# Kernel optimization log

Hardware: AMD Instinct MI355X
Metric: run time of the kernel (lower is better)

The kernel has to match this reference:

```python
import jax, jax.numpy as jnp
import numpy as np

B, S, D, H = 2, 2048, 1024, 16
HD = D // H


def setup_inputs() -> dict:
    key = jax.random.key(0)
    ks = jax.random.split(key, 5)
    scale = 0.02
    x = jax.random.normal(ks[0], (B, S, D), dtype=jnp.float32)
    Wq = jax.random.normal(ks[1], (D, D), dtype=jnp.float32) * scale
    Wk = jax.random.normal(ks[2], (D, D), dtype=jnp.float32) * scale
    Wv = jax.random.normal(ks[3], (D, D), dtype=jnp.float32) * scale
    Wo = jax.random.normal(ks[4], (D, D), dtype=jnp.float32) * scale
    z = jnp.zeros((D,), dtype=jnp.float32)
    return {"x": x, "Wq": Wq, "bq": z, "Wk": Wk, "bk": z, "Wv": Wv, "bv": z, "Wo": Wo, "bo": z}


def reference(x, Wq, bq, Wk, bk, Wv, bv, Wo, bo):
    b, s, d = x.shape
    hd = d // H
    # QKV projections -> [b, H, s, hd]
    def heads(W, bias):
        return (x @ W.T + bias).reshape(b, s, H, hd).transpose(0, 2, 1, 3)
    q = heads(Wq, bq)
    k = heads(Wk, bk)
    v = heads(Wv, bv)
    scale = 1.0 / np.sqrt(hd).astype(np.float32)
    attn = scale * jnp.einsum('bhqd,bhkd->bhqk', q, k)  # [b,H,s,s]
    # causal mask (attn dropout p=0 is identity before masking)
    causal = jnp.tril(jnp.ones((s, s), dtype=bool))
    attn = jnp.where(causal[None, None], attn, -jnp.inf)
    attn = jax.nn.softmax(attn, axis=-1)
    ans = jnp.einsum('bhqk,bhkd->bhqd', attn, v)
    ans = ans.transpose(0, 2, 1, 3).reshape(b, s, d)
    return ans @ Wo.T + bo
```

## Files before the change

### kernel.cpp

```cpp
#include <hip/hip_runtime.h>

#define DEV __device__ __forceinline__

typedef __attribute__((ext_vector_type(8))) __bf16 bf16x8;
typedef __attribute__((ext_vector_type(4))) float f32x4;
typedef __attribute__((ext_vector_type(16))) float f32x16;
typedef __attribute__((ext_vector_type(4))) unsigned short u16x4;
typedef __attribute__((ext_vector_type(8))) unsigned short u16x8;
typedef __attribute__((ext_vector_type(2))) unsigned u32x2;

DEV unsigned short f2bf(float f) {
  unsigned u = __builtin_bit_cast(unsigned, f);
  u += 0x7FFFu + ((u >> 16) & 1u);
  return (unsigned short)(u >> 16);
}

DEV f32x4 mfma16(bf16x8 a, bf16x8 b, f32x4 c) {
  return __builtin_amdgcn_mfma_f32_16x16x32_bf16(a, b, c, 0, 0, 0);
}
DEV f32x16 mfma32(bf16x8 a, bf16x8 b, f32x16 c) {
  return __builtin_amdgcn_mfma_f32_32x32x16_bf16(a, b, c, 0, 0, 0);
}

DEV void gload16(const void* g, void* l) {
  __builtin_amdgcn_global_load_lds(
      (const __attribute__((address_space(1))) unsigned int*)g,
      (__attribute__((address_space(3))) unsigned int*)l, 16, 0, 0);
}

DEV void plswap(unsigned& x, unsigned& y) {
#if __has_builtin(__builtin_amdgcn_permlane32_swap)
  u32x2 r = __builtin_amdgcn_permlane32_swap(x, y, false, false);
  x = r[0];
  y = r[1];
#else
  unsigned sx = __shfl_xor(x, 32, 64), sy = __shfl_xor(y, 32, 64);
  int hi = (threadIdx.x & 63) >> 5;
  unsigned nx = hi ? sy : x;
  unsigned ny = hi ? y : sx;
  x = nx;
  y = ny;
#endif
}
DEV float xadd32(float v) {
  unsigned a = __builtin_bit_cast(unsigned, v), b = a;
  plswap(a, b);
  return __builtin_bit_cast(float, a) + __builtin_bit_cast(float, b);
}

__global__ __launch_bounds__(256) void k_cvt_all(
    const float* __restrict__ x,
    const float* __restrict__ Wq, const float* __restrict__ Wk,
    const float* __restrict__ Wv, const float* __restrict__ Wo,
    unsigned short* __restrict__ xb,
    unsigned short* __restrict__ Wqb, unsigned short* __restrict__ Wkb,
    unsigned short* __restrict__ Wvb, unsigned short* __restrict__ Wob) {
  int g = blockIdx.x * 256 + threadIdx.x;
  const float* src;
  unsigned short* dst;
  int loc;
  if (g < 524288) {
    src = x; dst = xb; loc = g;
  } else {
    int r = g - 524288;
    int w = r >> 17;
    loc = r & 131071;
    src = w == 0 ? Wq : w == 1 ? Wk : w == 2 ? Wv : Wo;
    dst = w == 0 ? Wqb : w == 1 ? Wkb : w == 2 ? Wvb : Wob;
  }
  int row = loc >> 7, k8 = loc & 127;
  const f32x4* s = (const f32x4*)(src + ((size_t)row << 10) + (k8 << 3));
  f32x4 a = s[0], b = s[1];
  u16x8 o;
  o[0] = f2bf(a[0]); o[1] = f2bf(a[1]); o[2] = f2bf(a[2]); o[3] = f2bf(a[3]);
  o[4] = f2bf(b[0]); o[5] = f2bf(b[1]); o[6] = f2bf(b[2]); o[7] = f2bf(b[3]);
  *(u16x8*)(dst + ((size_t)row << 10) + ((k8 << 3) ^ ((row & 7) << 3))) = o;
}

DEV void gemm_mainloop(const char* Ag, const char* Bg, char* lds,
                       int lane, int wid, f32x4 acc[4][4]) {
  int g4 = lane >> 4, r16 = lane & 15;
  int wm = wid >> 1, wn = wid & 1;
  int adA[2], adB[2];
#pragma unroll
  for (int ks = 0; ks < 2; ++ks) {
    int swz = ((ks * 4 + g4) ^ (lane & 7)) << 4;
    adA[ks] = (wm * 64 + r16) * 128 + swz;
    adB[ks] = 16384 + (wn * 64 + r16) * 128 + swz;
  }
  int o0 = wid * 4096 + lane * 16;
  int grow[4], ginr[4];
#pragma unroll
  for (int i = 0; i < 4; ++i) {
    grow[i] = (o0 + i * 1024) >> 7;
    ginr[i] = (o0 + i * 1024) & 127;
  }
  auto STAGE = [&](int KT, int BASE) {
#pragma unroll
    for (int i = 0; i < 4; ++i) {
      int oo = o0 + i * 1024;
      size_t gofs = (size_t)grow[i] * 2048 + (size_t)KT * 128 + ginr[i];
      gload16(Ag + gofs, lds + BASE + oo);
      gload16(Bg + gofs, lds + BASE + 16384 + oo);
    }
  };
  STAGE(0, 0);
  __syncthreads();
  for (int kt = 0; kt < 16; ++kt) {
    int cur = (kt & 1) << 15;
    if (kt + 1 < 16) STAGE(kt + 1, cur ^ 32768);
#pragma unroll
    for (int ks = 0; ks < 2; ++ks) {
      bf16x8 af[4], bfr[4];
#pragma unroll
      for (int i = 0; i < 4; ++i) {
        af[i]  = *(const bf16x8*)(lds + cur + adA[ks] + i * 2048);
        bfr[i] = *(const bf16x8*)(lds + cur + adB[ks] + i * 2048);
      }
#pragma unroll
      for (int mi = 0; mi < 4; ++mi)
#pragma unroll
        for (int ni = 0; ni < 4; ++ni)
          acc[mi][ni] = mfma16(af[mi], bfr[ni], acc[mi][ni]);
    }
    __syncthreads();
  }
}

__global__ __launch_bounds__(256) void k_gemm_qkv(
    const unsigned short* __restrict__ xb,
    const unsigned short* __restrict__ Wqb, const unsigned short* __restrict__ Wkb,
    const unsigned short* __restrict__ Wvb,
    const float* __restrict__ bq, const float* __restrict__ bk,
    const float* __restrict__ bv,
    unsigned short* __restrict__ Qb, unsigned short* __restrict__ Kb,
    unsigned short* __restrict__ Vt) {
  __shared__ char lds[65536];
  int tid = threadIdx.x, lane = tid & 63, wid = tid >> 6;
  int bm = blockIdx.x & 31, bn = blockIdx.x >> 5;
  int r0 = bm * 128;
  int colT = bn * 128;
  int which = colT >> 10;
  int ncol = colT & 1023;
  const unsigned short* Wb = which == 0 ? Wqb : which == 1 ? Wkb : Wvb;
  f32x4 acc[4][4] = {};
  gemm_mainloop((const char*)xb + (size_t)r0 * 2048,
                (const char*)Wb + (size_t)ncol * 2048, lds, lane, wid, acc);
  int g4 = lane >> 4, r16 = lane & 15, wm = wid >> 1, wn = wid & 1;
  const float* bias = which == 0 ? bq : which == 1 ? bk : bv;
  int ncolw = ncol + wn * 64;
#pragma unroll
  for (int ni = 0; ni < 4; ++ni) {
    int gcol = ncolw + ni * 16 + r16;
    float bvv = bias[gcol];
    int h = gcol >> 6, hd = gcol & 63;
#pragma unroll
    for (int mi = 0; mi < 4; ++mi) {
      int growb = r0 + wm * 64 + mi * 16 + g4 * 4;
      int bb = growb >> 11, s0 = growb & 2047;
      if (which == 2) {
        u16x4 pk;
#pragma unroll
        for (int jj = 0; jj < 4; ++jj) pk[jj] = f2bf(acc[mi][ni][jj] + bvv);
        *(u16x4*)(Vt + ((size_t)(bb * 16 + h) * 64 + hd) * 2048 + s0) = pk;
      } else {
        unsigned short* dst = which == 0 ? Qb : Kb;
        size_t base = ((size_t)(bb * 16 + h) * 2048 + s0) * 64 + hd;
#pragma unroll
        for (int jj = 0; jj < 4; ++jj)
          dst[base + (size_t)jj * 64] = f2bf(acc[mi][ni][jj] + bvv);
      }
    }
  }
}

__global__ __launch_bounds__(256) void k_attn(
    const unsigned short* __restrict__ Q, const unsigned short* __restrict__ K,
    const unsigned short* __restrict__ Vt, unsigned short* __restrict__ ansb) {
  __shared__ char lds[3 * 16384 + 512];
  const float SCL = 0.18033688f;
  int tid = threadIdx.x, lane = tid & 63, wid = tid >> 6;
  int l31 = lane & 31, hi = lane >> 5;
  int bid = blockIdx.x;
  int bh = (bid & 7) * 4 + ((bid >> 3) & 3);
  int g = bid >> 5;
  int chunk = g < 8 ? 15 - g : g - 8;
  int b = bh >> 4, h = bh & 15;
  int q0 = chunk * 128 + wid * 32;
  int nt = 2 * chunk + 2;
  const unsigned short* Qh = Q + (size_t)bh * (2048 * 64);
  const char* Kg = (const char*)(K + (size_t)bh * (2048 * 64));
  const char* Vg = (const char*)(Vt + (size_t)bh * (64 * 2048));
  char* wb = lds + 49152 + wid * 128;

  int ldo0 = tid * 16, ldo1 = tid * 16 + 4096;
  int row0 = ldo0 >> 7, c0 = ldo0 & 127;
  int row1 = ldo1 >> 7, c1 = ldo1 & 127;
  int sc0 = c0 ^ ((row0 & 7) << 4), sc1 = c1 ^ ((row1 & 7) << 4);
  int ko0 = row0 * 128 + sc0, ko1 = row1 * 128 + sc1;
  int vo0 = row0 * 4096 + sc0, vo1 = row1 * 4096 + sc1;

  bf16x8 qf[4];
#pragma unroll
  for (int ks = 0; ks < 4; ++ks)
    qf[ks] = *(const bf16x8*)(Qh + (size_t)(q0 + l31) * 64 + ks * 16 + hi * 8);
  asm volatile("s_waitcnt vmcnt(0)" ::: "memory");

  f32x16 O0 = {}, O1 = {}, l16 = {};
  int swzl = (l31 & 7) << 4;
  int hioff = hi * 16;

  gload16(Kg + ko0, lds + ldo0);
  gload16(Kg + ko1, lds + ldo1);
  gload16(Vg + vo0, lds + 8192 + ldo0);
  gload16(Vg + vo1, lds + 8192 + ldo1);
  gload16(Kg + (size_t)64 * 128 + ko0, lds + 16384 + ldo0);
  gload16(Kg + (size_t)64 * 128 + ko1, lds + 16384 + ldo1);
  gload16(Vg + (size_t)64 * 2 + vo0, lds + 16384 + 8192 + ldo0);
  gload16(Vg + (size_t)64 * 2 + vo1, lds + 16384 + 8192 + ldo1);

  int cur = 0;
  for (int t = 0; t < nt; ++t) {
    if (t + 1 < nt) {
      asm volatile("s_waitcnt vmcnt(8)" ::: "memory");
    } else {
      asm volatile("s_waitcnt vmcnt(0)" ::: "memory");
    }
    __builtin_amdgcn_s_barrier();
    __builtin_amdgcn_sched_barrier(0);
    if (t + 2 < nt) {
      size_t kv2 = (size_t)(t + 2) * 64;
      int pb = (cur + 2 >= 3 ? cur - 1 : cur + 2) * 16384;
      gload16(Kg + kv2 * 128 + ko0, lds + pb + ldo0);
      gload16(Kg + kv2 * 128 + ko1, lds + pb + ldo1);
      gload16(Vg + kv2 * 2 + vo0, lds + pb + 8192 + ldo0);
      gload16(Vg + kv2 * 2 + vo1, lds + pb + 8192 + ldo1);
    }
    int kv0 = t * 64;
    if (kv0 <= q0 + 31) {
      const char* KL = lds + cur * 16384;
      const char* VL = KL + 8192;
      f32x16 s0 = {}, s1 = {};
      __builtin_amdgcn_s_setprio(1);
#pragma unroll
      for (int ks = 0; ks < 4; ++ks) {
        bf16x8 kf0 = *(const bf16x8*)(KL + l31 * 128 + ((ks * 32 + hioff) ^ swzl));
        bf16x8 kf1 = *(const bf16x8*)(KL + (32 + l31) * 128 + ((ks * 32 + hioff) ^ swzl));
        s0 = mfma32(kf0, qf[ks], s0);
        s1 = mfma32(kf1, qf[ks], s1);
      }
      __builtin_amdgcn_s_setprio(0);
      if (kv0 + 63 > q0) {
        int lim2 = q0 + l31 - kv0 - 4 * hi;
#pragma unroll
        for (int r = 0; r < 16; ++r) {
          int kc = (r & 3) + 8 * (r >> 2);
          if (kc > lim2) s0[r] = -1e30f;
          if (kc + 32 > lim2) s1[r] = -1e30f;
        }
      }
#pragma unroll
      for (int r = 0; r < 16; ++r) {
        s0[r] = __builtin_amdgcn_exp2f(s0[r] * SCL);
        s1[r] = __builtin_amdgcn_exp2f(s1[r] * SCL);
        l16[r] += s0[r] + s1[r];
      }
      __builtin_amdgcn_s_setprio(1);
#define PV_CHUNK(SV, E, C16) { \
      unsigned x0, x1, y0, y1; \
      asm("v_cvt_pk_bf16_f32 %0, %1, %2" : "=v"(x0) : "v"(SV[8*(E)+0]), "v"(SV[8*(E)+1])); \
      asm("v_cvt_pk_bf16_f32 %0, %1, %2" : "=v"(x1) : "v"(SV[8*(E)+2]), "v"(SV[8*(E)+3])); \
      asm("v_cvt_pk_bf16_f32 %0, %1, %2" : "=v"(y0) : "v"(SV[8*(E)+4]), "v"(SV[8*(E)+5])); \
      asm("v_cvt_pk_bf16_f32 %0, %1, %2" : "=v"(y1) : "v"(SV[8*(E)+6]), "v"(SV[8*(E)+7])); \
      plswap(x0, y0); \
      plswap(x1, y1); \
      union { unsigned u[4]; bf16x8 v; } pf; \
      pf.u[0] = x0; \
      pf.u[1] = x1; \
      pf.u[2] = y0; \
      pf.u[3] = y1; \
      bf16x8 v0 = *(const bf16x8*)(VL + l31 * 128 + (((C16) * 32 + hioff) ^ swzl)); \
      bf16x8 v1 = *(const bf16x8*)(VL + (32 + l31) * 128 + (((C16) * 32 + hioff) ^ swzl)); \
      O0 = mfma32(pf.v, v0, O0); \
      O1 = mfma32(pf.v, v1, O1); }
      PV_CHUNK(s0, 0, 0)
      PV_CHUNK(s0, 1, 1)
      PV_CHUNK(s1, 0, 2)
      PV_CHUNK(s1, 1, 3)
#undef PV_CHUNK
      __builtin_amdgcn_s_setprio(0);
    }
    cur = cur + 1 == 3 ? 0 : cur + 1;
  }
  float a[16];
#pragma unroll
  for (int r = 0; r < 16; ++r) a[r] = l16[r];
#pragma unroll
  for (int st2 = 8; st2 >= 1; st2 >>= 1)
#pragma unroll
    for (int i = 0; i < st2; ++i) a[i] += a[i + st2];
  float lf = xadd32(a[0]);
  float rl = 1.f / lf;
  if (lane < 32) *(float*)(wb + l31 * 4) = rl;
  asm volatile("s_waitcnt lgkmcnt(0)" ::: "memory");
  f32x4 rv0 = *(const f32x4*)(wb + hioff);
  f32x4 rv1 = *(const f32x4*)(wb + 32 + hioff);
  f32x4 rv2 = *(const f32x4*)(wb + 64 + hioff);
  f32x4 rv3 = *(const f32x4*)(wb + 96 + hioff);
#pragma unroll
  for (int r = 0; r < 16; ++r) {
    float sc = (r < 4 ? rv0 : r < 8 ? rv1 : r < 12 ? rv2 : rv3)[r & 3];
    int rowl = q0 + (r & 3) + 8 * (r >> 2) + 4 * hi;
    int rowg = (b << 11) + rowl;
    int cswz = (rowl & 7) << 3;
    int cg0 = (h << 6) + l31;
    int cg1 = (h << 6) + 32 + l31;
    ansb[(size_t)rowg * 1024 + (cg0 ^ cswz)] = f2bf(O0[r] * sc);
    ansb[(size_t)rowg * 1024 + (cg1 ^ cswz)] = f2bf(O1[r] * sc);
  }
}

__global__ __launch_bounds__(256) void k_gemm_out(
    const unsigned short* __restrict__ ansb, const unsigned short* __restrict__ Wob,
    const float* __restrict__ bo, float* __restrict__ out) {
  __shared__ char lds[65536];
  int tid = threadIdx.x, lane = tid & 63, wid = tid >> 6;
  int bm = blockIdx.x & 31, bn = blockIdx.x >> 5;
  int r0 = bm * 128, c0 = bn * 128;
  f32x4 acc[4][4] = {};
  gemm_mainloop((const char*)ansb + (size_t)r0 * 2048,
                (const char*)Wob + (size_t)c0 * 2048, lds, lane, wid, acc);
  int g4 = lane >> 4, r16 = lane & 15, wm = wid >> 1, wn = wid & 1;
#pragma unroll
  for (int ni = 0; ni < 4; ++ni) {
    int gcol = c0 + wn * 64 + ni * 16 + r16;
    float bvv = bo[gcol];
#pragma unroll
    for (int mi = 0; mi < 4; ++mi) {
      int growb = r0 + wm * 64 + mi * 16 + g4 * 4;
#pragma unroll
      for (int jj = 0; jj < 4; ++jj)
        out[(size_t)(growb + jj) * 1024 + gcol] = acc[mi][ni][jj] + bvv;
    }
  }
}

extern "C" void kernel_launch(void* const* d_in, const int* in_sizes, int n_in,
                              void* d_out, int out_size, void* d_ws, size_t ws_size,
                              hipStream_t stream) {
  const float* x  = (const float*)d_in[0];
  const float* Wq = (const float*)d_in[1];
  const float* bq = (const float*)d_in[2];
  const float* Wk = (const float*)d_in[3];
  const float* bk = (const float*)d_in[4];
  const float* Wv = (const float*)d_in[5];
  const float* bv = (const float*)d_in[6];
  const float* Wo = (const float*)d_in[7];
  const float* bo = (const float*)d_in[8];
  char* ws = (char*)d_ws;
  unsigned short* xb   = (unsigned short*)(ws);
  unsigned short* ansb = (unsigned short*)(ws);
  unsigned short* Wqb  = (unsigned short*)(ws + (8u  << 20));
  unsigned short* Wkb  = (unsigned short*)(ws + (10u << 20));
  unsigned short* Wvb  = (unsigned short*)(ws + (12u << 20));
  unsigned short* Wob  = (unsigned short*)(ws + (14u << 20));
  unsigned short* Qb   = (unsigned short*)(ws + (16u << 20));
  unsigned short* Kb   = (unsigned short*)(ws + (24u << 20));
  unsigned short* Vt   = (unsigned short*)(ws + (32u << 20));

  k_cvt_all<<<4096, 256, 0, stream>>>(x, Wq, Wk, Wv, Wo, xb, Wqb, Wkb, Wvb, Wob);
  k_gemm_qkv<<<768, 256, 0, stream>>>(xb, Wqb, Wkb, Wvb, bq, bk, bv, Qb, Kb, Vt);
  k_attn<<<512, 256, 0, stream>>>(Qb, Kb, Vt, ansb);
  k_gemm_out<<<256, 256, 0, stream>>>(ansb, Wob, bo, (float*)d_out);
}
```

Measured before the change: 107.1 us.

## Halve attention block size, fold softmax scale into Q, double-buffer KV

The attention kernel now runs 1024 blocks of 2 waves covering 64 query rows each, up from 512 blocks of 4 waves covering 128 rows. Chunk ordering is reshuffled for causal load balance. The 3-stage LDS ring with explicit vmcnt waits becomes a 2-stage double buffer with __syncthreads, and per-tile skipping of fully masked tiles goes away. The softmax scale is folded into Q in the QKV GEMM epilogue, which removes a multiply per score. The trade is more parallelism and smaller LDS use per block against a shallower prefetch pipeline and more block-level barriers.

```diff
diff --git a/kernel.cpp b/kernel.cpp
--- a/kernel.cpp
+++ b/kernel.cpp
@@ -148,6 +148,7 @@
                 (const char*)Wb + (size_t)ncol * 2048, lds, lane, wid, acc);
   int g4 = lane >> 4, r16 = lane & 15, wm = wid >> 1, wn = wid & 1;
   const float* bias = which == 0 ? bq : which == 1 ? bk : bv;
+  float oscale = which == 0 ? 0.18033688f : 1.0f;
   int ncolw = ncol + wn * 64;
 #pragma unroll
   for (int ni = 0; ni < 4; ++ni) {
@@ -168,129 +169,118 @@
         size_t base = ((size_t)(bb * 16 + h) * 2048 + s0) * 64 + hd;
 #pragma unroll
         for (int jj = 0; jj < 4; ++jj)
-          dst[base + (size_t)jj * 64] = f2bf(acc[mi][ni][jj] + bvv);
+          dst[base + (size_t)jj * 64] = f2bf((acc[mi][ni][jj] + bvv) * oscale);
       }
     }
   }
 }
 
-__global__ __launch_bounds__(256) void k_attn(
+__global__ __launch_bounds__(128) void k_attn(
     const unsigned short* __restrict__ Q, const unsigned short* __restrict__ K,
     const unsigned short* __restrict__ Vt, unsigned short* __restrict__ ansb) {
-  __shared__ char lds[3 * 16384 + 512];
-  const float SCL = 0.18033688f;
+  __shared__ char lds[2 * 16384 + 256];
   int tid = threadIdx.x, lane = tid & 63, wid = tid >> 6;
   int l31 = lane & 31, hi = lane >> 5;
   int bid = blockIdx.x;
   int bh = (bid & 7) * 4 + ((bid >> 3) & 3);
   int g = bid >> 5;
-  int chunk = g < 8 ? 15 - g : g - 8;
+  int chunk = g < 8 ? g : g < 16 ? 39 - g : g < 24 ? 31 - g : g - 8;
   int b = bh >> 4, h = bh & 15;
-  int q0 = chunk * 128 + wid * 32;
-  int nt = 2 * chunk + 2;
+  int q0 = chunk * 64 + wid * 32;
+  int nt = chunk + 1;
   const unsigned short* Qh = Q + (size_t)bh * (2048 * 64);
   const char* Kg = (const char*)(K + (size_t)bh * (2048 * 64));
   const char* Vg = (const char*)(Vt + (size_t)bh * (64 * 2048));
-  char* wb = lds + 49152 + wid * 128;
-
-  int ldo0 = tid * 16, ldo1 = tid * 16 + 4096;
-  int row0 = ldo0 >> 7, c0 = ldo0 & 127;
-  int row1 = ldo1 >> 7, c1 = ldo1 & 127;
-  int sc0 = c0 ^ ((row0 & 7) << 4), sc1 = c1 ^ ((row1 & 7) << 4);
-  int ko0 = row0 * 128 + sc0, ko1 = row1 * 128 + sc1;
-  int vo0 = row0 * 4096 + sc0, vo1 = row1 * 4096 + sc1;
+  char* wb = lds + 32768 + wid * 128;
+
+  int kof[4], ko[4], vo[4];
+#pragma unroll
+  for (int i = 0; i < 4; ++i) {
+    int o = tid * 16 + i * 2048;
+    int row = o >> 7, c = o & 127;
+    int sc = c ^ ((row & 7) << 4);
+    kof[i] = o;
+    ko[i] = row * 128 + sc;
+    vo[i] = row * 4096 + sc;
+  }
 
   bf16x8 qf[4];
 #pragma unroll
   for (int ks = 0; ks < 4; ++ks)
     qf[ks] = *(const bf16x8*)(Qh + (size_t)(q0 + l31) * 64 + ks * 16 + hi * 8);
-  asm volatile("s_waitcnt vmcnt(0)" ::: "memory");
 
   f32x16 O0 = {}, O1 = {}, l16 = {};
   int swzl = (l31 & 7) << 4;
   int hioff = hi * 16;
 
-  gload16(Kg + ko0, lds + ldo0);
-  gload16(Kg + ko1, lds + ldo1);
-  gload16(Vg + vo0, lds + 8192 + ldo0);
-  gload16(Vg + vo1, lds + 8192 + ldo1);
-  gload16(Kg + (size_t)64 * 128 + ko0, lds + 16384 + ldo0);
-  gload16(Kg + (size_t)64 * 128 + ko1, lds + 16384 + ldo1);
-  gload16(Vg + (size_t)64 * 2 + vo0, lds + 16384 + 8192 + ldo0);
-  gload16(Vg + (size_t)64 * 2 + vo1, lds + 16384 + 8192 + ldo1);
-
-  int cur = 0;
+  auto STAGEA = [&](int T, int BASE) {
+    size_t kK = (size_t)T * 8192;
+    size_t kV = (size_t)T * 128;
+#pragma unroll
+    for (int i = 0; i < 4; ++i) {
+      gload16(Kg + kK + ko[i], lds + BASE + kof[i]);
+      gload16(Vg + kV + vo[i], lds + BASE + 8192 + kof[i]);
+    }
+  };
+
+  STAGEA(0, 0);
+  __syncthreads();
   for (int t = 0; t < nt; ++t) {
-    if (t + 1 < nt) {
-      asm volatile("s_waitcnt vmcnt(8)" ::: "memory");
-    } else {
-      asm volatile("s_waitcnt vmcnt(0)" ::: "memory");
-    }
-    __builtin_amdgcn_s_barrier();
-    __builtin_amdgcn_sched_barrier(0);
-    if (t + 2 < nt) {
-      size_t kv2 = (size_t)(t + 2) * 64;
-      int pb = (cur + 2 >= 3 ? cur - 1 : cur + 2) * 16384;
-      gload16(Kg + kv2 * 128 + ko0, lds + pb + ldo0);
-      gload16(Kg + kv2 * 128 + ko1, lds + pb + ldo1);
-      gload16(Vg + kv2 * 2 + vo0, lds + pb + 8192 + ldo0);
-      gload16(Vg + kv2 * 2 + vo1, lds + pb + 8192 + ldo1);
-    }
+    int cur = (t & 1) << 14;
+    if (t + 1 < nt) STAGEA(t + 1, cur ^ 16384);
+    const char* KL = lds + cur;
+    const char* VL = KL + 8192;
     int kv0 = t * 64;
-    if (kv0 <= q0 + 31) {
-      const char* KL = lds + cur * 16384;
-      const char* VL = KL + 8192;
-      f32x16 s0 = {}, s1 = {};
-      __builtin_amdgcn_s_setprio(1);
-#pragma unroll
-      for (int ks = 0; ks < 4; ++ks) {
-        bf16x8 kf0 = *(const bf16x8*)(KL + l31 * 128 + ((ks * 32 + hioff) ^ swzl));
-        bf16x8 kf1 = *(const bf16x8*)(KL + (32 + l31) * 128 + ((ks * 32 + hioff) ^ swzl));
-        s0 = mfma32(kf0, qf[ks], s0);
-        s1 = mfma32(kf1, qf[ks], s1);
+    f32x16 s0 = {}, s1 = {};
+    __builtin_amdgcn_s_setprio(1);
+#pragma unroll
+    for (int ks = 0; ks < 4; ++ks) {
+      bf16x8 kf0 = *(const bf16x8*)(KL + l31 * 128 + ((ks * 32 + hioff) ^ swzl));
+      bf16x8 kf1 = *(const bf16x8*)(KL + (32 + l31) * 128 + ((ks * 32 + hioff) ^ swzl));
+      s0 = mfma32(kf0, qf[ks], s0);
+      s1 = mfma32(kf1, qf[ks], s1);
+    }
+    __builtin_amdgcn_s_setprio(0);
+    if (kv0 + 63 > q0) {
+      int lim2 = q0 + l31 - kv0 - 4 * hi;
+#pragma unroll
+      for (int r = 0; r < 16; ++r) {
+        int kc = (r & 3) + 8 * (r >> 2);
+        if (kc > lim2) s0[r] = -1e30f;
+        if (kc + 32 > lim2) s1[r] = -1e30f;
       }
-      __builtin_amdgcn_s_setprio(0);
-      if (kv0 + 63 > q0) {
-        int lim2 = q0 + l31 - kv0 - 4 * hi;
-#pragma unroll
-        for (int r = 0; r < 16; ++r) {
-          int kc = (r & 3) + 8 * (r >> 2);
-          if (kc > lim2) s0[r] = -1e30f;
-          if (kc + 32 > lim2) s1[r] = -1e30f;
-        }
-      }
-#pragma unroll
-      for (int r = 0; r < 16; ++r) {
-        s0[r] = __builtin_amdgcn_exp2f(s0[r] * SCL);
-        s1[r] = __builtin_amdgcn_exp2f(s1[r] * SCL);
-        l16[r] += s0[r] + s1[r];
-      }
-      __builtin_amdgcn_s_setprio(1);
+    }
+#pragma unroll
+    for (int r = 0; r < 16; ++r) {
+      s0[r] = __builtin_amdgcn_exp2f(s0[r]);
+      s1[r] = __builtin_amdgcn_exp2f(s1[r]);
+      l16[r] += s0[r] + s1[r];
+    }
+    __builtin_amdgcn_s_setprio(1);
 #define PV_CHUNK(SV, E, C16) { \
-      unsigned x0, x1, y0, y1; \
-      asm("v_cvt_pk_bf16_f32 %0, %1, %2" : "=v"(x0) : "v"(SV[8*(E)+0]), "v"(SV[8*(E)+1])); \
-      asm("v_cvt_pk_bf16_f32 %0, %1, %2" : "=v"(x1) : "v"(SV[8*(E)+2]), "v"(SV[8*(E)+3])); \
-      asm("v_cvt_pk_bf16_f32 %0, %1, %2" : "=v"(y0) : "v"(SV[8*(E)+4]), "v"(SV[8*(E)+5])); \
-      asm("v_cvt_pk_bf16_f32 %0, %1, %2" : "=v"(y1) : "v"(SV[8*(E)+6]), "v"(SV[8*(E)+7])); \
-      plswap(x0, y0); \
-      plswap(x1, y1); \
-      union { unsigned u[4]; bf16x8 v; } pf; \
-      pf.u[0] = x0; \
-      pf.u[1] = x1; \
-      pf.u[2] = y0; \
-      pf.u[3] = y1; \
-      bf16x8 v0 = *(const bf16x8*)(VL + l31 * 128 + (((C16) * 32 + hioff) ^ swzl)); \
-      bf16x8 v1 = *(const bf16x8*)(VL + (32 + l31) * 128 + (((C16) * 32 + hioff) ^ swzl)); \
-      O0 = mfma32(pf.v, v0, O0); \
-      O1 = mfma32(pf.v, v1, O1); }
-      PV_CHUNK(s0, 0, 0)
-      PV_CHUNK(s0, 1, 1)
-      PV_CHUNK(s1, 0, 2)
-      PV_CHUNK(s1, 1, 3)
+    unsigned x0, x1, y0, y1; \
+    asm("v_cvt_pk_bf16_f32 %0, %1, %2" : "=v"(x0) : "v"(SV[8*(E)+0]), "v"(SV[8*(E)+1])); \
+    asm("v_cvt_pk_bf16_f32 %0, %1, %2" : "=v"(x1) : "v"(SV[8*(E)+2]), "v"(SV[8*(E)+3])); \
+    asm("v_cvt_pk_bf16_f32 %0, %1, %2" : "=v"(y0) : "v"(SV[8*(E)+4]), "v"(SV[8*(E)+5])); \
+    asm("v_cvt_pk_bf16_f32 %0, %1, %2" : "=v"(y1) : "v"(SV[8*(E)+6]), "v"(SV[8*(E)+7])); \
+    plswap(x0, y0); \
+    plswap(x1, y1); \
+    union { unsigned u[4]; bf16x8 v; } pf; \
+    pf.u[0] = x0; \
+    pf.u[1] = x1; \
+    pf.u[2] = y0; \
+    pf.u[3] = y1; \
+    bf16x8 v0 = *(const bf16x8*)(VL + l31 * 128 + (((C16) * 32 + hioff) ^ swzl)); \
+    bf16x8 v1 = *(const bf16x8*)(VL + (32 + l31) * 128 + (((C16) * 32 + hioff) ^ swzl)); \
+    O0 = mfma32(pf.v, v0, O0); \
+    O1 = mfma32(pf.v, v1, O1); }
+    PV_CHUNK(s0, 0, 0)
+    PV_CHUNK(s0, 1, 1)
+    PV_CHUNK(s1, 0, 2)
+    PV_CHUNK(s1, 1, 3)
 #undef PV_CHUNK
-      __builtin_amdgcn_s_setprio(0);
-    }
-    cur = cur + 1 == 3 ? 0 : cur + 1;
+    __builtin_amdgcn_s_setprio(0);
+    __syncthreads();
   }
   float a[16];
 #pragma unroll
@@ -370,6 +360,6 @@
 
   k_cvt_all<<<4096, 256, 0, stream>>>(x, Wq, Wk, Wv, Wo, xb, Wqb, Wkb, Wvb, Wob);
   k_gemm_qkv<<<768, 256, 0, stream>>>(xb, Wqb, Wkb, Wvb, bq, bk, bv, Qb, Kb, Vt);
-  k_attn<<<512, 256, 0, stream>>>(Qb, Kb, Vt, ansb);
+  k_attn<<<1024, 128, 0, stream>>>(Qb, Kb, Vt, ansb);
   k_gemm_out<<<256, 256, 0, stream>>>(ansb, Wob, bo, (float*)d_out);
 }
```

Result: no change. 108.4 us (+1.2%).
